# Kernel optimization log

Measured on AMD Instinct MI355X. Metric: run time of the kernel, lower is better.

The kernel has to match this reference:

```python
import jax, jax.numpy as jnp
import numpy as np

# Dimensions (see shape_source)
L = 1024   # episode_len (memory slots)
B = 64     # batch (parallel envs)
K = 512    # key_size
V = 512    # value_size
H = 8      # num_head
MEMB = 256 # memory_state_embedding
SDIM = 512 # state_dim
HID = 512  # hidden width of all 2-layer encoders
RIMQ = 512 # rim_query_size
LAT = K - MEMB  # task_inference_latent dim


def setup_inputs() -> dict:
    key = jax.random.key(0)
    ks = jax.random.split(key, 16)
    w = lambda k, shape: (jax.random.normal(k, shape, jnp.float32) * 0.02)
    return {
        "state": jax.random.normal(ks[0], (B, SDIM), jnp.float32),
        "task_inference_latent": jax.random.normal(ks[1], (B, LAT), jnp.float32),
        "keys": jax.random.normal(ks[2], (L, B, K), jnp.float32),
        "vals": jax.random.normal(ks[3], (L, B, V), jnp.float32),
        "rpe_mod": jax.random.uniform(ks[4], (L, B, 1), jnp.float32),
        "step": jnp.maximum(jax.random.randint(ks[5], (B,), 0, L), 1),
        "W_state": w(ks[6], (SDIM, MEMB)), "b_state": jnp.zeros((MEMB,), jnp.float32),
        "Wcq1": w(ks[7], (K, HID)), "bcq1": jnp.zeros((HID,), jnp.float32),
        "Wcq2": w(ks[8], (HID, K)), "bcq2": jnp.zeros((K,), jnp.float32),
        "Wq": w(ks[9], (K, H * K)), "bq": jnp.zeros((H * K,), jnp.float32),
        "Wagg": w(ks[10], (H * V, V)), "bagg": jnp.zeros((V,), jnp.float32),
        "Wrk1": w(ks[11], (V, HID)), "brk1": jnp.zeros((HID,), jnp.float32),
        "Wrk2": w(ks[12], (HID, RIMQ)), "brk2": jnp.zeros((RIMQ,), jnp.float32),
        "Wrv1": w(ks[13], (V, HID)), "brv1": jnp.zeros((HID,), jnp.float32),
        "Wrv2": w(ks[14], (HID, V)), "brv2": jnp.zeros((V,), jnp.float32),
    }


def reference(state, task_inference_latent, keys, vals, rpe_mod, step,
              W_state, b_state, Wcq1, bcq1, Wcq2, bcq2, Wq, bq, Wagg, bagg,
              Wrk1, brk1, Wrk2, brk2, Wrv1, brv1, Wrv2, brv2):
    # DND.read (exploration branch), vectorized over the batch loop.
    se = state @ W_state + b_state                         # state_encoder: [B, MEMB]
    q = jnp.concatenate([se, task_inference_latent], -1)   # [B, K]
    # concat_query_encoder: stacked Linears with NO nonlinearity (faithful to source)
    q = (q @ Wcq1 + bcq1) @ Wcq2 + bcq2                    # [B, K]
    q = (q @ Wq + bq).reshape(B, H, K)                     # multi-head queries

    mk = keys * rpe_mod                                    # RPE-modulated keys [L, B, K]
    scores = jnp.einsum('lbk,bhk->blh', mk, q) / jnp.sqrt(jnp.float32(K))  # [B, L, H]
    valid = jnp.arange(L)[None, :] < step[:, None]         # [B, L] only slots < step[i]
    scores = jnp.where(valid[:, :, None], scores, jnp.float32(-1e30))
    prob = jax.nn.softmax(scores, axis=1) * valid[:, :, None].astype(scores.dtype)

    result = jnp.einsum('blh,lbv->bhv', prob, vals).reshape(B, H * V)
    result = (result @ Wagg + bagg)[:, None, :]            # value_aggregator -> [B, 1, V]
    out_key = (result @ Wrk1 + brk1) @ Wrk2 + brk2         # read_memory_to_key  [B, 1, RIMQ]
    out_val = (result @ Wrv1 + brv1) @ Wrv2 + brv2         # read_memory_to_value [B, 1, V]
    return out_key, out_val
```

## Files before the change

### kernel.cpp

```cpp
#include <hip/hip_runtime.h>
#include <math.h>

#define F4(p)  (*reinterpret_cast<float4*>(p))
#define CF4(p) (*reinterpret_cast<const float4*>(p))

#define NCHUNK 16

__device__ __forceinline__ void gemm_core(
    const float* __restrict__ Asrc, const float* __restrict__ inbias,
    const float* __restrict__ til,
    int NS, int srcld, int kc, int k0,
    const float* __restrict__ W, int ldw, int n0,
    const float* __restrict__ obias, float* __restrict__ Pout, int ldo)
{
    __shared__ float As[16*64], Ws[16*64];
    const int t = threadIdx.x;
    const int tx = t & 15, ty = t >> 4;
    const int row = t >> 2, kq = (t & 3) * 4;
    const int wrow = t >> 4, wcol = (t & 15) * 4;
    float acc[4][4] = {};
    for (int kk = 0; kk < kc; kk += 16) {
        const int kg = k0 + kk + kq;
        float4 av;
        if (til && kg >= 256) {
            av = CF4(&til[row*256 + (kg - 256)]);
        } else {
            av = {0.f, 0.f, 0.f, 0.f};
            if (inbias) av = CF4(&inbias[kg]);
            for (int s = 0; s < NS; ++s) {
                float4 v = CF4(&Asrc[(size_t)(s*64 + row)*srcld + kg]);
                av.x += v.x; av.y += v.y; av.z += v.z; av.w += v.w;
            }
        }
        As[(kq+0)*64+row] = av.x; As[(kq+1)*64+row] = av.y;
        As[(kq+2)*64+row] = av.z; As[(kq+3)*64+row] = av.w;
        F4(&Ws[wrow*64 + wcol]) = CF4(&W[(size_t)(k0 + kk + wrow)*ldw + n0 + wcol]);
        __syncthreads();
        #pragma unroll
        for (int k = 0; k < 16; ++k) {
            float4 a4 = CF4(&As[k*64 + ty*4]);
            float4 w4 = CF4(&Ws[k*64 + tx*4]);
            float a[4] = {a4.x, a4.y, a4.z, a4.w};
            float w[4] = {w4.x, w4.y, w4.z, w4.w};
            #pragma unroll
            for (int i = 0; i < 4; ++i)
                #pragma unroll
                for (int j = 0; j < 4; ++j)
                    acc[i][j] += a[i] * w[j];
        }
        __syncthreads();
    }
    #pragma unroll
    for (int i = 0; i < 4; ++i) {
        float4 o = {acc[i][0], acc[i][1], acc[i][2], acc[i][3]};
        if (obias) {
            float4 ob = CF4(&obias[n0 + tx*4]);
            o.x += ob.x; o.y += ob.y; o.z += ob.z; o.w += ob.w;
        }
        F4(&Pout[(size_t)(ty*4 + i)*ldo + n0 + tx*4]) = o;
    }
}

__global__ __launch_bounds__(256) void k_q1(
    const float* __restrict__ state, const float* __restrict__ W_state,
    float* __restrict__ P1)
{
    const int nt = blockIdx.x, ks = blockIdx.y;
    gemm_core(state, nullptr, nullptr, 1, 512, 64, ks*64,
              W_state, 256, nt*64, nullptr, P1 + (size_t)ks*64*256, 256);
}

__global__ __launch_bounds__(256) void k_q2(
    const float* __restrict__ P1, const float* __restrict__ b_state,
    const float* __restrict__ til, const float* __restrict__ Wcq1,
    float* __restrict__ P2)
{
    const int nt = blockIdx.x, ks = blockIdx.y;
    gemm_core(P1, b_state, til, 8, 256, 64, ks*64,
              Wcq1, 512, nt*64, nullptr, P2 + (size_t)ks*64*512, 512);
}

__global__ __launch_bounds__(256) void k_q3(
    const float* __restrict__ P2, const float* __restrict__ bcq1,
    const float* __restrict__ Wcq2, float* __restrict__ P3)
{
    const int nt = blockIdx.x, ks = blockIdx.y;
    gemm_core(P2, bcq1, nullptr, 8, 512, 64, ks*64,
              Wcq2, 512, nt*64, nullptr, P3 + (size_t)ks*64*512, 512);
}

__global__ __launch_bounds__(256) void k_qh(
    const float* __restrict__ P3, const float* __restrict__ bcq2,
    const float* __restrict__ Wq, float* __restrict__ P4)
{
    const int nt = blockIdx.x, ks = blockIdx.y;
    gemm_core(P3, bcq2, nullptr, 8, 512, 128, ks*128,
              Wq, 4096, nt*64, nullptr, P4 + (size_t)ks*64*4096, 4096);
}

__global__ __launch_bounds__(256) void k_qsum(
    const float* __restrict__ P4, const float* __restrict__ bq,
    float* __restrict__ qh)
{
    const int b = blockIdx.x, t = threadIdx.x;
    #pragma unroll
    for (int j = 0; j < 4; ++j) {
        int f = t + j*256;
        float4 v = CF4(&bq[f*4]);
        #pragma unroll
        for (int s = 0; s < 4; ++s) {
            float4 u = CF4(&P4[(size_t)(s*64 + b)*4096 + f*4]);
            v.x += u.x; v.y += u.y; v.z += u.z; v.w += u.w;
        }
        F4(&qh[(size_t)b*4096 + f*4]) = v;
    }
}

__global__ __launch_bounds__(256, 4) void k_fa(
    const float* __restrict__ keys, const float* __restrict__ rpe,
    const float* __restrict__ qh, const float* __restrict__ vals,
    const int* __restrict__ step,
    float* __restrict__ Facc, float* __restrict__ Fms)
{
    __shared__ float s_q[4096];
    __shared__ float s_kt[2][2048];
    __shared__ float s_sc[64*8];
    __shared__ float s_rpe[64];
    __shared__ float red[256];
    __shared__ float s_m[8];
    const int b = blockIdx.y, lc = blockIdx.x;
    const int sb = step[b];
    const int l0 = (lc * sb) / NCHUNK;
    const int l1 = ((lc + 1) * sb) / NCHUNK;
    const int nl = l1 - l0;
    const int t = threadIdx.x;
    float* facc_out = Facc + ((size_t)(lc*64) + b)*4096;
    if (nl <= 0) {
        float4 z = {0.f, 0.f, 0.f, 0.f};
        for (int i = t; i < 1024; i += 256) F4(&facc_out[i*4]) = z;
        if (t < 8) {
            size_t o = ((size_t)(lc*64 + b)*8 + t)*2;
            Fms[o] = -1e30f; Fms[o+1] = 0.f;
        }
        return;
    }
    const int ntile = (nl + 3) >> 2;
    const int j0 = t, j1 = t + 256;
    const int r0 = j0 >> 7, c0 = (j0 & 127) * 4;
    const int r1 = j1 >> 7, c1 = (j1 & 127) * 4;
    const float inv_sqrtK = 0.04419417382415922f;

    {
        int la = min(l0 + r0, sb - 1), lb = min(l0 + r1, sb - 1);
        float4 ra = CF4(&keys[((size_t)la*64 + b)*512 + c0]);
        float4 rb = CF4(&keys[((size_t)lb*64 + b)*512 + c1]);
        for (int i = t; i < 1024; i += 256)
            F4(&s_q[i*4]) = CF4(&qh[(size_t)b*4096 + i*4]);
        if (t < nl) s_rpe[t] = rpe[(l0 + t)*64 + b] * inv_sqrtK;
        F4(&s_kt[0][j0*4]) = ra;
        F4(&s_kt[0][j1*4]) = rb;
    }
    __syncthreads();

    const int lane = t & 63, w = t >> 6;
    const bool p0 = lane & 1, p1 = lane & 2, p2 = lane & 4;
    for (int i = 0; i < ntile; ++i) {
        const int cur = i & 1;
        float4 ra, rb;
        const bool more = (i + 1 < ntile);
        if (more) {
            int la = min(l0 + (i+1)*4 + r0, sb - 1);
            int lb = min(l0 + (i+1)*4 + r1, sb - 1);
            ra = CF4(&keys[((size_t)la*64 + b)*512 + c0]);
            rb = CF4(&keys[((size_t)lb*64 + b)*512 + c1]);
        }
        const int r = i*4 + w;
        if (r < nl) {
            float4 kx = CF4(&s_kt[cur][w*512 + lane*8]);
            float4 ky = CF4(&s_kt[cur][w*512 + lane*8 + 4]);
            float kv[8] = {kx.x,kx.y,kx.z,kx.w, ky.x,ky.y,ky.z,ky.w};
            float pr[8] = {};
            #pragma unroll
            for (int h = 0; h < 8; ++h) {
                float4 qx = CF4(&s_q[h*512 + lane*8]);
                float4 qy = CF4(&s_q[h*512 + lane*8 + 4]);
                pr[h] = kv[0]*qx.x + kv[1]*qx.y + kv[2]*qx.z + kv[3]*qx.w
                      + kv[4]*qy.x + kv[5]*qy.y + kv[6]*qy.z + kv[7]*qy.w;
            }
            float w4[4], x2[2], y;
            #pragma unroll
            for (int q = 0; q < 4; ++q) {
                float keep = p0 ? pr[2*q+1] : pr[2*q];
                float send = p0 ? pr[2*q]   : pr[2*q+1];
                w4[q] = keep + __shfl_xor(send, 1);
            }
            #pragma unroll
            for (int q = 0; q < 2; ++q) {
                float keep = p1 ? w4[2*q+1] : w4[2*q];
                float send = p1 ? w4[2*q]   : w4[2*q+1];
                x2[q] = keep + __shfl_xor(send, 2);
            }
            {
                float keep = p2 ? x2[1] : x2[0];
                float send = p2 ? x2[0] : x2[1];
                y = keep + __shfl_xor(send, 4);
            }
            y += __shfl_xor(y, 8);
            y += __shfl_xor(y, 16);
            y += __shfl_xor(y, 32);
            if (lane < 8)
                s_sc[r*8 + lane] = y * s_rpe[r];
        }
        __syncthreads();
        if (more) {
            F4(&s_kt[cur ^ 1][j0*4]) = ra;
            F4(&s_kt[cur ^ 1][j1*4]) = rb;
        }
        __syncthreads();
    }
    const int h = t & 7, g = t >> 3;
    float m = -1e30f;
    for (int l = g; l < nl; l += 32) m = fmaxf(m, s_sc[l*8 + h]);
    red[g*8 + h] = m;
    __syncthreads();
    #pragma unroll
    for (int s = 16; s; s >>= 1) {
        if (g < s) red[g*8+h] = fmaxf(red[g*8+h], red[(g+s)*8+h]);
        __syncthreads();
    }
    if (t < 8) s_m[t] = red[t];
    __syncthreads();
    float mh = s_m[h], s_acc = 0.f;
    for (int l = g; l < nl; l += 32) {
        float e = __expf(s_sc[l*8 + h] - mh);
        s_sc[l*8 + h] = e;
        s_acc += e;
    }
    red[g*8 + h] = s_acc;
    __syncthreads();
    #pragma unroll
    for (int s = 16; s; s >>= 1) {
        if (g < s) red[g*8+h] += red[(g+s)*8+h];
        __syncthreads();
    }
    if (t < 8) {
        size_t o = ((size_t)(lc*64 + b)*8 + t)*2;
        Fms[o] = s_m[t]; Fms[o+1] = red[t];
    }
    __syncthreads();
    const int par = t >> 7, c = t & 127;
    float4 acc[8] = {};
    {
        int la = min(l0 + r0, sb - 1), lb = min(l0 + r1, sb - 1);
        float4 ra = CF4(&vals[((size_t)la*64 + b)*512 + c0]);
        float4 rb = CF4(&vals[((size_t)lb*64 + b)*512 + c1]);
        F4(&s_kt[0][j0*4]) = ra;
        F4(&s_kt[0][j1*4]) = rb;
    }
    __syncthreads();
    for (int i = 0; i < ntile; ++i) {
        const int cur = i & 1;
        float4 ra, rb;
        const bool more = (i + 1 < ntile);
        if (more) {
            int la = min(l0 + (i+1)*4 + r0, sb - 1);
            int lb = min(l0 + (i+1)*4 + r1, sb - 1);
            ra = CF4(&vals[((size_t)la*64 + b)*512 + c0]);
            rb = CF4(&vals[((size_t)lb*64 + b)*512 + c1]);
        }
        #pragma unroll
        for (int sub = 0; sub < 2; ++sub) {
            const int tr = par + sub*2;
            const int row = i*4 + tr;
            if (row < nl) {
                float4 v = CF4(&s_kt[cur][tr*512 + c*4]);
                float4 pa = CF4(&s_sc[row*8]);
                float4 pb = CF4(&s_sc[row*8 + 4]);
                acc[0].x += pa.x*v.x; acc[0].y += pa.x*v.y; acc[0].z += pa.x*v.z; acc[0].w += pa.x*v.w;
                acc[1].x += pa.y*v.x; acc[1].y += pa.y*v.y; acc[1].z += pa.y*v.z; acc[1].w += pa.y*v.w;
                acc[2].x += pa.z*v.x; acc[2].y += pa.z*v.y; acc[2].z += pa.z*v.z; acc[2].w += pa.z*v.w;
                acc[3].x += pa.w*v.x; acc[3].y += pa.w*v.y; acc[3].z += pa.w*v.z; acc[3].w += pa.w*v.w;
                acc[4].x += pb.x*v.x; acc[4].y += pb.x*v.y; acc[4].z += pb.x*v.z; acc[4].w += pb.x*v.w;
                acc[5].x += pb.y*v.x; acc[5].y += pb.y*v.y; acc[5].z += pb.y*v.z; acc[5].w += pb.y*v.w;
                acc[6].x += pb.z*v.x; acc[6].y += pb.z*v.y; acc[6].z += pb.z*v.z; acc[6].w += pb.z*v.w;
                acc[7].x += pb.w*v.x; acc[7].y += pb.w*v.y; acc[7].z += pb.w*v.z; acc[7].w += pb.w*v.w;
            }
        }
        __syncthreads();
        if (more) {
            F4(&s_kt[cur ^ 1][j0*4]) = ra;
            F4(&s_kt[cur ^ 1][j1*4]) = rb;
        }
        __syncthreads();
    }
    if (par == 1) {
        #pragma unroll
        for (int hh = 0; hh < 8; ++hh)
            F4(&s_q[(c*8 + hh)*4]) = acc[hh];
    }
    __syncthreads();
    if (par == 0) {
        #pragma unroll
        for (int hh = 0; hh < 8; ++hh) {
            float4 o = CF4(&s_q[(c*8 + hh)*4]);
            o.x += acc[hh].x; o.y += acc[hh].y; o.z += acc[hh].z; o.w += acc[hh].w;
            F4(&facc_out[hh*512 + c*4]) = o;
        }
    }
}

__global__ __launch_bounds__(256) void k_comb(
    const float* __restrict__ Facc, const float* __restrict__ Fms,
    float* __restrict__ res)
{
    __shared__ float wgt[NCHUNK*8];
    const int b = blockIdx.x, t = threadIdx.x;
    if (t < 8) {
        float mm[NCHUNK], ss[NCHUNK], e[NCHUNK];
        float M = -1e30f;
        #pragma unroll
        for (int i = 0; i < NCHUNK; ++i) {
            size_t o = ((size_t)(i*64 + b)*8 + t)*2;
            mm[i] = Fms[o]; ss[i] = Fms[o+1];
            M = fmaxf(M, mm[i]);
        }
        float D = 0.f;
        #pragma unroll
        for (int i = 0; i < NCHUNK; ++i) { e[i] = __expf(mm[i] - M); D += e[i]*ss[i]; }
        float invD = 1.f / D;
        #pragma unroll
        for (int i = 0; i < NCHUNK; ++i) wgt[i*8 + t] = e[i] * invD;
    }
    __syncthreads();
    #pragma unroll
    for (int j = 0; j < 4; ++j) {
        int f = t + j*256;
        int h = f >> 7;
        float4 a = {0.f, 0.f, 0.f, 0.f};
        #pragma unroll
        for (int i = 0; i < NCHUNK; ++i) {
            float wi = wgt[i*8 + h];
            float4 v = CF4(&Facc[((size_t)(i*64) + b)*4096 + f*4]);
            a.x += wi*v.x; a.y += wi*v.y; a.z += wi*v.z; a.w += wi*v.w;
        }
        F4(&res[(size_t)b*4096 + f*4]) = a;
    }
}

__global__ __launch_bounds__(256) void k_agg(
    const float* __restrict__ res, const float* __restrict__ Wagg,
    float* __restrict__ P5)
{
    const int nt = blockIdx.x, ks = blockIdx.y;
    gemm_core(res, nullptr, nullptr, 1, 4096, 128, ks*128,
              Wagg, 512, nt*64, nullptr, P5 + (size_t)ks*64*512, 512);
}

__global__ __launch_bounds__(256) void k_rkv1(
    const float* __restrict__ P5, const float* __restrict__ bagg,
    const float* __restrict__ Wrk1, const float* __restrict__ Wrv1,
    float* __restrict__ P6)
{
    const int nt = blockIdx.x, ks = blockIdx.y, z = blockIdx.z;
    gemm_core(P5, bagg, nullptr, 32, 512, 128, ks*128,
              z ? Wrv1 : Wrk1, 512, nt*64,
              nullptr, P6 + (size_t)(z*4 + ks)*64*512, 512);
}

__global__ __launch_bounds__(256) void k_rkv2(
    const float* __restrict__ P6,
    const float* __restrict__ brk1, const float* __restrict__ brv1,
    const float* __restrict__ Wrk2, const float* __restrict__ Wrv2,
    const float* __restrict__ brk2, const float* __restrict__ brv2,
    float* __restrict__ out)
{
    const int nt = blockIdx.x, z = blockIdx.z;
    gemm_core(P6 + (size_t)z*4*64*512, z ? brv1 : brk1, nullptr, 4, 512, 512, 0,
              z ? Wrv2 : Wrk2, 512, nt*64,
              z ? brv2 : brk2, out + (size_t)z*64*512, 512);
}

extern "C" void kernel_launch(void* const* d_in, const int* in_sizes, int n_in,
                              void* d_out, int out_size, void* d_ws, size_t ws_size,
                              hipStream_t stream) {
    const float* state   = (const float*)d_in[0];
    const float* til     = (const float*)d_in[1];
    const float* keys    = (const float*)d_in[2];
    const float* vals    = (const float*)d_in[3];
    const float* rpe     = (const float*)d_in[4];
    const int*   step    = (const int*)d_in[5];
    const float* W_state = (const float*)d_in[6];
    const float* b_state = (const float*)d_in[7];
    const float* Wcq1 = (const float*)d_in[8];
    const float* bcq1 = (const float*)d_in[9];
    const float* Wcq2 = (const float*)d_in[10];
    const float* bcq2 = (const float*)d_in[11];
    const float* Wq   = (const float*)d_in[12];
    const float* bq   = (const float*)d_in[13];
    const float* Wagg = (const float*)d_in[14];
    const float* bagg = (const float*)d_in[15];
    const float* Wrk1 = (const float*)d_in[16];
    const float* brk1 = (const float*)d_in[17];
    const float* Wrk2 = (const float*)d_in[18];
    const float* brk2 = (const float*)d_in[19];
    const float* Wrv1 = (const float*)d_in[20];
    const float* brv1 = (const float*)d_in[21];
    const float* Wrv2 = (const float*)d_in[22];
    const float* brv2 = (const float*)d_in[23];
    float* out = (float*)d_out;
    float* ws  = (float*)d_ws;

    float* P1   = ws;
    float* P2   = ws + 131072;
    float* P3   = ws + 393216;
    float* P4   = ws + 655360;
    float* qh   = ws + 1703936;
    float* Facc = ws + 1966080;
    float* Fms  = ws + 6160384;
    float* res  = ws + 6176768;
    float* P5   = ws;
    float* P6   = ws + 1048576;

    k_q1  <<<dim3(4,8),   256, 0, stream>>>(state, W_state, P1);
    k_q2  <<<dim3(8,8),   256, 0, stream>>>(P1, b_state, til, Wcq1, P2);
    k_q3  <<<dim3(8,8),   256, 0, stream>>>(P2, bcq1, Wcq2, P3);
    k_qh  <<<dim3(64,4),  256, 0, stream>>>(P3, bcq2, Wq, P4);
    k_qsum<<<64, 256, 0, stream>>>(P4, bq, qh);
    k_fa  <<<dim3(NCHUNK,64), 256, 0, stream>>>(keys, rpe, qh, vals, step, Facc, Fms);
    k_comb<<<64, 256, 0, stream>>>(Facc, Fms, res);
    k_agg <<<dim3(8,32),  256, 0, stream>>>(res, Wagg, P5);
    k_rkv1<<<dim3(8,4,2), 256, 0, stream>>>(P5, bagg, Wrk1, Wrv1, P6);
    k_rkv2<<<dim3(8,1,2), 256, 0, stream>>>(P6, brk1, brv1, Wrk2, Wrv2,
                                            brk2, brv2, out);
}
```

Before: 166.9 us.

## Stream keys/vals straight into registers and drop shared-memory staging and barriers

The flash-attention chunk kernel no longer stages key and value tiles through double-buffered shared memory with two barriers per tile. Each wave now loads its own key rows from global memory into registers with a two-deep software prefetch, and the query heads are held in registers (64 floats per thread) instead of shared memory. The value pass also reads rows directly per thread-half with register prefetch. This removes most __syncthreads and LDS traffic, at the cost of much higher register pressure that may cut occupancy under launch_bounds(256,4).

```diff
diff --git a/kernel.cpp b/kernel.cpp
--- a/kernel.cpp
+++ b/kernel.cpp
@@ -122,8 +122,7 @@
     const int* __restrict__ step,
     float* __restrict__ Facc, float* __restrict__ Fms)
 {
-    __shared__ float s_q[4096];
-    __shared__ float s_kt[2][2048];
+    __shared__ float s_cmb[4096];
     __shared__ float s_sc[64*8];
     __shared__ float s_rpe[64];
     __shared__ float red[256];
@@ -144,80 +143,79 @@
         }
         return;
     }
-    const int ntile = (nl + 3) >> 2;
-    const int j0 = t, j1 = t + 256;
-    const int r0 = j0 >> 7, c0 = (j0 & 127) * 4;
-    const int r1 = j1 >> 7, c1 = (j1 & 127) * 4;
     const float inv_sqrtK = 0.04419417382415922f;
-
+    if (t < nl) s_rpe[t] = rpe[(l0 + t)*64 + b] * inv_sqrtK;
+    __syncthreads();
+
+    const int lane = t & 63, w = t >> 6;
+    float qr[8][8];
     {
-        int la = min(l0 + r0, sb - 1), lb = min(l0 + r1, sb - 1);
-        float4 ra = CF4(&keys[((size_t)la*64 + b)*512 + c0]);
-        float4 rb = CF4(&keys[((size_t)lb*64 + b)*512 + c1]);
-        for (int i = t; i < 1024; i += 256)
-            F4(&s_q[i*4]) = CF4(&qh[(size_t)b*4096 + i*4]);
-        if (t < nl) s_rpe[t] = rpe[(l0 + t)*64 + b] * inv_sqrtK;
-        F4(&s_kt[0][j0*4]) = ra;
-        F4(&s_kt[0][j1*4]) = rb;
-    }
-    __syncthreads();
-
-    const int lane = t & 63, w = t >> 6;
+        const float* qb = qh + (size_t)b*4096 + lane*8;
+        #pragma unroll
+        for (int h = 0; h < 8; ++h) {
+            float4 x = CF4(&qb[h*512]);
+            float4 y = CF4(&qb[h*512 + 4]);
+            qr[h][0]=x.x; qr[h][1]=x.y; qr[h][2]=x.z; qr[h][3]=x.w;
+            qr[h][4]=y.x; qr[h][5]=y.y; qr[h][6]=y.z; qr[h][7]=y.w;
+        }
+    }
     const bool p0 = lane & 1, p1 = lane & 2, p2 = lane & 4;
-    for (int i = 0; i < ntile; ++i) {
-        const int cur = i & 1;
-        float4 ra, rb;
-        const bool more = (i + 1 < ntile);
-        if (more) {
-            int la = min(l0 + (i+1)*4 + r0, sb - 1);
-            int lb = min(l0 + (i+1)*4 + r1, sb - 1);
-            ra = CF4(&keys[((size_t)la*64 + b)*512 + c0]);
-            rb = CF4(&keys[((size_t)lb*64 + b)*512 + c1]);
-        }
-        const int r = i*4 + w;
-        if (r < nl) {
-            float4 kx = CF4(&s_kt[cur][w*512 + lane*8]);
-            float4 ky = CF4(&s_kt[cur][w*512 + lane*8 + 4]);
-            float kv[8] = {kx.x,kx.y,kx.z,kx.w, ky.x,ky.y,ky.z,ky.w};
-            float pr[8] = {};
+    const size_t RS = (size_t)64*512;
+
+    auto score_row = [&](float4 kx, float4 ky, int r) {
+        float kv[8] = {kx.x,kx.y,kx.z,kx.w, ky.x,ky.y,ky.z,ky.w};
+        float pr[8] = {};
+        #pragma unroll
+        for (int h = 0; h < 8; ++h)
             #pragma unroll
-            for (int h = 0; h < 8; ++h) {
-                float4 qx = CF4(&s_q[h*512 + lane*8]);
-                float4 qy = CF4(&s_q[h*512 + lane*8 + 4]);
-                pr[h] = kv[0]*qx.x + kv[1]*qx.y + kv[2]*qx.z + kv[3]*qx.w
-                      + kv[4]*qy.x + kv[5]*qy.y + kv[6]*qy.z + kv[7]*qy.w;
+            for (int j = 0; j < 8; ++j)
+                pr[h] += kv[j] * qr[h][j];
+        float w4[4], x2[2], y;
+        #pragma unroll
+        for (int q = 0; q < 4; ++q) {
+            float keep = p0 ? pr[2*q+1] : pr[2*q];
+            float send = p0 ? pr[2*q]   : pr[2*q+1];
+            w4[q] = keep + __shfl_xor(send, 1);
+        }
+        #pragma unroll
+        for (int q = 0; q < 2; ++q) {
+            float keep = p1 ? w4[2*q+1] : w4[2*q];
+            float send = p1 ? w4[2*q]   : w4[2*q+1];
+            x2[q] = keep + __shfl_xor(send, 2);
+        }
+        {
+            float keep = p2 ? x2[1] : x2[0];
+            float send = p2 ? x2[0] : x2[1];
+            y = keep + __shfl_xor(send, 4);
+        }
+        y += __shfl_xor(y, 8);
+        y += __shfl_xor(y, 16);
+        y += __shfl_xor(y, 32);
+        if (lane < 8) s_sc[r*8 + lane] = y * s_rpe[r];
+    };
+
+    {
+        const float* kpA = keys + ((size_t)(l0 + w)*64 + b)*512 + lane*8;
+        const float* kpB = kpA + 4*RS;
+        float4 A0x, A0y, A1x, A1y, B0x, B0y, B1x, B1y;
+        if (w < nl)      { A0x = CF4(kpA);        A0y = CF4(kpA + 4); }
+        if (w + 4 < nl)  { B0x = CF4(kpB);        B0y = CF4(kpB + 4); }
+        if (w + 8 < nl)  { A1x = CF4(kpA + 8*RS); A1y = CF4(kpA + 8*RS + 4); }
+        if (w + 12 < nl) { B1x = CF4(kpB + 8*RS); B1y = CF4(kpB + 8*RS + 4); }
+        for (int il = w; il < nl; il += 8) {
+            score_row(A0x, A0y, il);
+            A0x = A1x; A0y = A1y;
+            if (il + 16 < nl) { A1x = CF4(kpA + 16*RS); A1y = CF4(kpA + 16*RS + 4); }
+            kpA += 8*RS;
+            if (il + 4 < nl) {
+                score_row(B0x, B0y, il + 4);
+                B0x = B1x; B0y = B1y;
+                if (il + 20 < nl) { B1x = CF4(kpB + 16*RS); B1y = CF4(kpB + 16*RS + 4); }
+                kpB += 8*RS;
             }
-            float w4[4], x2[2], y;
-            #pragma unroll
-            for (int q = 0; q < 4; ++q) {
-                float keep = p0 ? pr[2*q+1] : pr[2*q];
-                float send = p0 ? pr[2*q]   : pr[2*q+1];
-                w4[q] = keep + __shfl_xor(send, 1);
-            }
-            #pragma unroll
-            for (int q = 0; q < 2; ++q) {
-                float keep = p1 ? w4[2*q+1] : w4[2*q];
-                float send = p1 ? w4[2*q]   : w4[2*q+1];
-                x2[q] = keep + __shfl_xor(send, 2);
-            }
-            {
-                float keep = p2 ? x2[1] : x2[0];
-                float send = p2 ? x2[0] : x2[1];
-                y = keep + __shfl_xor(send, 4);
-            }
-            y += __shfl_xor(y, 8);
-            y += __shfl_xor(y, 16);
-            y += __shfl_xor(y, 32);
-            if (lane < 8)
-                s_sc[r*8 + lane] = y * s_rpe[r];
-        }
-        __syncthreads();
-        if (more) {
-            F4(&s_kt[cur ^ 1][j0*4]) = ra;
-            F4(&s_kt[cur ^ 1][j1*4]) = rb;
-        }
-        __syncthreads();
-    }
+        }
+    }
+    __syncthreads();
     const int h = t & 7, g = t >> 3;
     float m = -1e30f;
     for (int l = g; l < nl; l += 32) m = fmaxf(m, s_sc[l*8 + h]);
@@ -247,62 +245,52 @@
         size_t o = ((size_t)(lc*64 + b)*8 + t)*2;
         Fms[o] = s_m[t]; Fms[o+1] = red[t];
     }
-    __syncthreads();
     const int par = t >> 7, c = t & 127;
     float4 acc[8] = {};
+    auto pv_row = [&](float4 v, int row) {
+        float4 pa = CF4(&s_sc[row*8]);
+        float4 pb = CF4(&s_sc[row*8 + 4]);
+        acc[0].x += pa.x*v.x; acc[0].y += pa.x*v.y; acc[0].z += pa.x*v.z; acc[0].w += pa.x*v.w;
+        acc[1].x += pa.y*v.x; acc[1].y += pa.y*v.y; acc[1].z += pa.y*v.z; acc[1].w += pa.y*v.w;
+        acc[2].x += pa.z*v.x; acc[2].y += pa.z*v.y; acc[2].z += pa.z*v.z; acc[2].w += pa.z*v.w;
+        acc[3].x += pa.w*v.x; acc[3].y += pa.w*v.y; acc[3].z += pa.w*v.z; acc[3].w += pa.w*v.w;
+        acc[4].x += pb.x*v.x; acc[4].y += pb.x*v.y; acc[4].z += pb.x*v.z; acc[4].w += pb.x*v.w;
+        acc[5].x += pb.y*v.x; acc[5].y += pb.y*v.y; acc[5].z += pb.y*v.z; acc[5].w += pb.y*v.w;
+        acc[6].x += pb.z*v.x; acc[6].y += pb.z*v.y; acc[6].z += pb.z*v.z; acc[6].w += pb.z*v.w;
+        acc[7].x += pb.w*v.x; acc[7].y += pb.w*v.y; acc[7].z += pb.w*v.z; acc[7].w += pb.w*v.w;
+    };
     {
-        int la = min(l0 + r0, sb - 1), lb = min(l0 + r1, sb - 1);
-        float4 ra = CF4(&vals[((size_t)la*64 + b)*512 + c0]);
-        float4 rb = CF4(&vals[((size_t)lb*64 + b)*512 + c1]);
-        F4(&s_kt[0][j0*4]) = ra;
-        F4(&s_kt[0][j1*4]) = rb;
-    }
-    __syncthreads();
-    for (int i = 0; i < ntile; ++i) {
-        const int cur = i & 1;
-        float4 ra, rb;
-        const bool more = (i + 1 < ntile);
-        if (more) {
-            int la = min(l0 + (i+1)*4 + r0, sb - 1);
-            int lb = min(l0 + (i+1)*4 + r1, sb - 1);
-            ra = CF4(&vals[((size_t)la*64 + b)*512 + c0]);
-            rb = CF4(&vals[((size_t)lb*64 + b)*512 + c1]);
-        }
-        #pragma unroll
-        for (int sub = 0; sub < 2; ++sub) {
-            const int tr = par + sub*2;
-            const int row = i*4 + tr;
-            if (row < nl) {
-                float4 v = CF4(&s_kt[cur][tr*512 + c*4]);
-                float4 pa = CF4(&s_sc[row*8]);
-                float4 pb = CF4(&s_sc[row*8 + 4]);
-                acc[0].x += pa.x*v.x; acc[0].y += pa.x*v.y; acc[0].z += pa.x*v.z; acc[0].w += pa.x*v.w;
-                acc[1].x += pa.y*v.x; acc[1].y += pa.y*v.y; acc[1].z += pa.y*v.z; acc[1].w += pa.y*v.w;
-                acc[2].x += pa.z*v.x; acc[2].y += pa.z*v.y; acc[2].z += pa.z*v.z; acc[2].w += pa.z*v.w;
-                acc[3].x += pa.w*v.x; acc[3].y += pa.w*v.y; acc[3].z += pa.w*v.z; acc[3].w += pa.w*v.w;
-                acc[4].x += pb.x*v.x; acc[4].y += pb.x*v.y; acc[4].z += pb.x*v.z; acc[4].w += pb.x*v.w;
-                acc[5].x += pb.y*v.x; acc[5].y += pb.y*v.y; acc[5].z += pb.y*v.z; acc[5].w += pb.y*v.w;
-                acc[6].x += pb.z*v.x; acc[6].y += pb.z*v.y; acc[6].z += pb.z*v.z; acc[6].w += pb.z*v.w;
-                acc[7].x += pb.w*v.x; acc[7].y += pb.w*v.y; acc[7].z += pb.w*v.z; acc[7].w += pb.w*v.w;
+        const float* vpA = vals + ((size_t)(l0 + par)*64 + b)*512 + c*4;
+        const float* vpB = vpA + 2*RS;
+        float4 VA0, VA1, VB0, VB1;
+        if (par < nl)     VA0 = CF4(vpA);
+        if (par + 2 < nl) VB0 = CF4(vpB);
+        if (par + 4 < nl) VA1 = CF4(vpA + 4*RS);
+        if (par + 6 < nl) VB1 = CF4(vpB + 4*RS);
+        for (int il = par; il < nl; il += 4) {
+            pv_row(VA0, il);
+            VA0 = VA1;
+            if (il + 8 < nl) VA1 = CF4(vpA + 8*RS);
+            vpA += 4*RS;
+            if (il + 2 < nl) {
+                pv_row(VB0, il + 2);
+                VB0 = VB1;
+                if (il + 10 < nl) VB1 = CF4(vpB + 8*RS);
+                vpB += 4*RS;
             }
         }
-        __syncthreads();
-        if (more) {
-            F4(&s_kt[cur ^ 1][j0*4]) = ra;
-            F4(&s_kt[cur ^ 1][j1*4]) = rb;
-        }
-        __syncthreads();
-    }
+    }
+    __syncthreads();
     if (par == 1) {
         #pragma unroll
         for (int hh = 0; hh < 8; ++hh)
-            F4(&s_q[(c*8 + hh)*4]) = acc[hh];
+            F4(&s_cmb[(c*8 + hh)*4]) = acc[hh];
     }
     __syncthreads();
     if (par == 0) {
         #pragma unroll
         for (int hh = 0; hh < 8; ++hh) {
-            float4 o = CF4(&s_q[(c*8 + hh)*4]);
+            float4 o = CF4(&s_cmb[(c*8 + hh)*4]);
             o.x += acc[hh].x; o.y += acc[hh].y; o.z += acc[hh].z; o.w += acc[hh].w;
             F4(&facc_out[hh*512 + c*4]) = o;
         }
```

Result: faster. 159.8 us (-4.3%).
